# Kernel optimization log

Measured on AMD Instinct MI355X. Metric: run time of the kernel, lower is better.

Reference implementation:

```python
import jax, jax.numpy as jnp
import numpy as np

SCALE = 0.02
EPS = 1e-5


def setup_inputs() -> dict:
    key = jax.random.key(0)
    ks = jax.random.split(key, 11)
    C = 256
    inp = {
        "x": jax.random.normal(ks[0], (64, C, 28, 28), dtype=jnp.float32),
        "w1": jax.random.normal(ks[1], (C, C, 3, 3), dtype=jnp.float32) * 0.05,
        "g1": jax.random.uniform(ks[2], (C,), dtype=jnp.float32, minval=0.5, maxval=1.5),
        "b1": jax.random.normal(ks[3], (C,), dtype=jnp.float32) * 0.1,
        "m1": jax.random.normal(ks[4], (C,), dtype=jnp.float32) * 0.1,
        "v1": jax.random.uniform(ks[5], (C,), dtype=jnp.float32, minval=0.5, maxval=1.5),
        "w2": jax.random.normal(ks[6], (C, C, 3, 3), dtype=jnp.float32) * 0.05,
        "g2": jax.random.uniform(ks[7], (C,), dtype=jnp.float32, minval=0.5, maxval=1.5),
        "b2": jax.random.normal(ks[8], (C,), dtype=jnp.float32) * 0.1,
        "m2": jax.random.normal(ks[9], (C,), dtype=jnp.float32) * 0.1,
        "v2": jax.random.uniform(ks[10], (C,), dtype=jnp.float32, minval=0.5, maxval=1.5),
    }
    return inp


def _bin_conv3x3(x, w, stride=1):
    # 1-bit weight conv: sign(w)*scale, straight-through estimator for grads.
    wb = w + jax.lax.stop_gradient(jnp.sign(w) - w)
    y = jax.lax.conv_general_dilated(
        x, wb,
        window_strides=(stride, stride),
        padding=[(1, 1), (1, 1)],
        dimension_numbers=("NCHW", "OIHW", "NCHW"),
    )
    return y * SCALE


def _bn(x, g, b, m, v):
    # eval-mode batchnorm with running stats
    inv = g * jax.lax.rsqrt(v + EPS)  # [C]
    return x * inv[None, :, None, None] + (b - m * inv)[None, :, None, None]


def reference(x, w1, g1, b1, m1, v1, w2, g2, b2, m2, v2):
    out = jax.nn.relu(_bn(_bin_conv3x3(x, w1, 1), g1, b1, m1, v1))
    out = _bn(_bin_conv3x3(out, w2, 1), g2, b2, m2, v2)
    return jax.nn.relu(out + x)
```

## Files before the change

kernel.cpp:

```cpp
#include <hip/hip_runtime.h>

#define EPS_F 1e-5f
#define SCALE_F 0.02f

using short8  = __attribute__((ext_vector_type(8))) short;
using floatx4 = __attribute__((ext_vector_type(4))) float;

__device__ __forceinline__ unsigned short f2bf(float f) {
  unsigned u = __float_as_uint(f);
  return (unsigned short)((u + 0x7fffu + ((u >> 16) & 1u)) >> 16);
}

__global__ void prep_w(const float* __restrict__ w1, const float* __restrict__ w2,
                       unsigned short* __restrict__ ap1, unsigned short* __restrict__ ap2,
                       const float* g1, const float* b1, const float* m1, const float* v1,
                       const float* g2, const float* b2, const float* m2, const float* v2,
                       float* bnp) {
  const float* __restrict__ w = blockIdx.y ? w2 : w1;
  unsigned short* __restrict__ ap = blockIdx.y ? ap2 : ap1;
  int t = blockIdx.x * 256 + threadIdx.x;
  int off = t >> 13;
  int c8  = (t >> 8) & 31;
  int co  = t & 255;
  const float* ws = w + (size_t)(co * 256 + c8 * 8) * 9 + off;
  short8 o;
#pragma unroll
  for (int j = 0; j < 8; ++j) {
    float v = ws[j * 9];
    o[j] = (v > 0.f) ? (short)0x3F80 : ((v < 0.f) ? (short)0xBF80 : (short)0);
  }
  *(short8*)(ap + (size_t)t * 8) = o;
  if (blockIdx.x == 0 && blockIdx.y == 0) {
    int c = threadIdx.x;
    float i1 = g1[c] * rsqrtf(v1[c] + EPS_F);
    bnp[c]       = SCALE_F * i1;
    bnp[256 + c] = b1[c] - m1[c] * i1;
    float i2 = g2[c] * rsqrtf(v2[c] + EPS_F);
    bnp[512 + c] = SCALE_F * i2;
    bnp[768 + c] = b2[c] - m2[c] * i2;
  }
}

__global__ void prep_x(const float* __restrict__ x, unsigned short* __restrict__ xb,
                       unsigned short* __restrict__ abuf) {
  __shared__ float tile[28 * 260];
  int h = blockIdx.x;
  int n = blockIdx.y;
  int tid = threadIdx.x;
  const float* xs = x + ((size_t)n * 256) * 784 + h * 28;
  for (int u = tid; u < 1792; u += 256) {
    int ci = u / 7;
    int j  = u - ci * 7;
    floatx4 f = *(const floatx4*)&xs[(size_t)ci * 784 + j * 4];
    tile[(j * 4 + 0) * 260 + ci] = f[0];
    tile[(j * 4 + 1) * 260 + ci] = f[1];
    tile[(j * 4 + 2) * 260 + ci] = f[2];
    tile[(j * 4 + 3) * 260 + ci] = f[3];
  }
  __syncthreads();
  unsigned short* xd = xb + ((size_t)n * 900 + (h + 1) * 30 + 1) * 256;
  for (int u = tid; u < 1792; u += 256) {
    int w  = u >> 6;
    int c4 = u & 63;
    floatx4 f = *(const floatx4*)&tile[w * 260 + c4 * 4];
    ushort4 o;
    o.x = f2bf(f[0]); o.y = f2bf(f[1]); o.z = f2bf(f[2]); o.w = f2bf(f[3]);
    *(ushort4*)(xd + (size_t)w * 256 + c4 * 4) = o;
  }
  {
    int bufi = tid >> 7, side = (tid >> 6) & 1, c4 = tid & 63;
    unsigned short* bb = (bufi ? abuf : xb) + ((size_t)n * 900 + (h + 1) * 30 + side * 29) * 256;
    ushort4 z = {0, 0, 0, 0};
    *(ushort4*)(bb + c4 * 4) = z;
  }
  if (h == 0 || h == 27) {
    int row = (h == 0) ? 0 : 29;
    for (int u = tid; u < 3840; u += 256) {
      int bufi = u / 1920;
      int r    = u - bufi * 1920;
      int px   = r >> 6, c4 = r & 63;
      unsigned short* bb = (bufi ? abuf : xb) + ((size_t)n * 900 + row * 30 + px) * 256;
      ushort4 z = {0, 0, 0, 0};
      *(ushort4*)(bb + c4 * 4) = z;
    }
  }
}

template<int STAGE>
__global__ __launch_bounds__(256, 2) void bconv(
    const unsigned short* __restrict__ Bin,
    const unsigned short* __restrict__ Apack,
    const float* __restrict__ bnp,
    unsigned short* __restrict__ aout,
    const float* __restrict__ xres,
    float* __restrict__ out)
{
  __shared__ __align__(16) unsigned short Blds[180 * 64];

  const int tid  = threadIdx.x;
  const int lane = tid & 63;
  const int wv   = tid >> 6;
  const int quad = lane >> 4;
  const int l16  = lane & 15;
  const int spBlk = blockIdx.x;
  const int n     = blockIdx.y;

  const int prow0 = 4 * spBlk;
  const unsigned short* bsrc = Bin + ((size_t)n * 900 + prow0 * 30) * 256;
  const int coW = wv * 64;

  int pxS[7];
#pragma unroll
  for (int s = 0; s < 7; ++s) {
    int lm = s * 16 + l16;
    int hl = lm / 28;
    int w  = lm - hl * 28;
    pxS[s] = hl * 30 + w;
  }

  floatx4 acc[4][7];
#pragma unroll
  for (int c = 0; c < 4; ++c)
#pragma unroll
    for (int s = 0; s < 7; ++s)
      acc[c][s] = (floatx4){0.f, 0.f, 0.f, 0.f};

#pragma unroll 1
  for (int cb = 0; cb < 4; ++cb) {
    __syncthreads();
    for (int u = tid; u < 1440; u += 256) {
      int px = u >> 3, c = u & 7;
      const unsigned short* src = bsrc + (size_t)px * 256 + cb * 64 + c * 8;
      *(short8*)&Blds[(px << 6) + ((c ^ (px & 7)) << 3)] = *(const short8*)src;
    }
    __syncthreads();

    const int cq = cb * 8 + quad;
#pragma unroll 1
    for (int kh = 0; kh < 3; ++kh) {
#pragma unroll 1
      for (int kw = 0; kw < 3; ++kw) {
        const int D = kh * 30 + kw;
        const int chunk0 = (kh * 3 + kw) * 32 + cq;
#pragma unroll
        for (int half = 0; half < 2; ++half) {
          const int chunk = chunk0 + half * 4;
          const unsigned short* apb = Apack + ((size_t)(chunk * 256 + coW + l16)) * 8;
          short8 a0 = *(const short8*)(apb);
          short8 a1 = *(const short8*)(apb + 16 * 8);
          short8 a2 = *(const short8*)(apb + 32 * 8);
          short8 a3 = *(const short8*)(apb + 48 * 8);
          const int C = half * 4 + quad;
#pragma unroll
          for (int s = 0; s < 7; ++s) {
            int pe = pxS[s] + D;
            short8 b = *(const short8*)&Blds[(pe << 6) + ((C ^ (pe & 7)) << 3)];
            acc[0][s] = __builtin_amdgcn_mfma_f32_16x16x32_bf16(a0, b, acc[0][s], 0, 0, 0);
            acc[1][s] = __builtin_amdgcn_mfma_f32_16x16x32_bf16(a1, b, acc[1][s], 0, 0, 0);
            acc[2][s] = __builtin_amdgcn_mfma_f32_16x16x32_bf16(a2, b, acc[2][s], 0, 0, 0);
            acc[3][s] = __builtin_amdgcn_mfma_f32_16x16x32_bf16(a3, b, acc[3][s], 0, 0, 0);
          }
        }
      }
    }
  }

  if (STAGE == 1) {
#pragma unroll
    for (int c = 0; c < 4; ++c) {
      int co = coW + c * 16 + quad * 4;
      floatx4 As = *(const floatx4*)(bnp + co);
      floatx4 Bs = *(const floatx4*)(bnp + 256 + co);
#pragma unroll
      for (int s = 0; s < 7; ++s) {
        int lm = s * 16 + l16;
        int hl = lm / 28;
        int w  = lm - hl * 28;
        int pix = (prow0 + hl + 1) * 30 + w + 1;
        unsigned short* dst = aout + ((size_t)n * 900 + pix) * 256 + co;
        ushort4 o;
        o.x = f2bf(fmaxf(acc[c][s][0] * As[0] + Bs[0], 0.f));
        o.y = f2bf(fmaxf(acc[c][s][1] * As[1] + Bs[1], 0.f));
        o.z = f2bf(fmaxf(acc[c][s][2] * As[2] + Bs[2], 0.f));
        o.w = f2bf(fmaxf(acc[c][s][3] * As[3] + Bs[3], 0.f));
        *(ushort4*)dst = o;
      }
    }
  } else {
#pragma unroll
    for (int c = 0; c < 4; ++c) {
      int co = coW + c * 16 + quad * 4;
      floatx4 As = *(const floatx4*)(bnp + 512 + co);
      floatx4 Bs = *(const floatx4*)(bnp + 768 + co);
#pragma unroll
      for (int s = 0; s < 7; ++s) {
        int m = spBlk * 112 + s * 16 + l16;
#pragma unroll
        for (int r = 0; r < 4; ++r) {
          size_t oidx = ((size_t)n * 256 + co + r) * 784 + m;
          float v = acc[c][s][r] * As[r] + Bs[r] + xres[oidx];
          out[oidx] = fmaxf(v, 0.f);
        }
      }
    }
  }
}


extern "C" void kernel_launch(void* const* d_in, const int* in_sizes, int n_in,
                              void* d_out, int out_size, void* d_ws, size_t ws_size,
                              hipStream_t stream) {
  const float* x  = (const float*)d_in[0];
  const float* w1 = (const float*)d_in[1];
  const float* g1 = (const float*)d_in[2];
  const float* b1 = (const float*)d_in[3];
  const float* m1 = (const float*)d_in[4];
  const float* v1 = (const float*)d_in[5];
  const float* w2 = (const float*)d_in[6];
  const float* g2 = (const float*)d_in[7];
  const float* b2 = (const float*)d_in[8];
  const float* m2 = (const float*)d_in[9];
  const float* v2 = (const float*)d_in[10];
  float* out = (float*)d_out;

  char* ws = (char*)d_ws;
  const size_t PADBUF = (size_t)64 * 900 * 256 * 2;
  const size_t WPACK  = 589824ull * 2;
  unsigned short* xb   = (unsigned short*)ws;
  unsigned short* abuf = (unsigned short*)(ws + PADBUF);
  unsigned short* ap1  = (unsigned short*)(ws + 2 * PADBUF);
  unsigned short* ap2  = (unsigned short*)(ws + 2 * PADBUF + WPACK);
  float* bnp           = (float*)(ws + 2 * PADBUF + 2 * WPACK);

  prep_w<<<dim3(288, 2), 256, 0, stream>>>(w1, w2, ap1, ap2,
                                           g1, b1, m1, v1, g2, b2, m2, v2, bnp);
  prep_x<<<dim3(28, 64), 256, 0, stream>>>(x, xb, abuf);

  dim3 grid(7, 64);
  bconv<1><<<grid, 256, 0, stream>>>(xb,   ap1, bnp, abuf, nullptr, nullptr);
  bconv<2><<<grid, 256, 0, stream>>>(abuf, ap2, bnp, nullptr, x, out);
}
```

Measured before the change: 264.0 us.

## Stage conv1 epilogue through LDS for coalesced stores, simplify prep_x transpose

The stage-1 epilogue now writes BN+ReLU bf16 results into a padded shared-memory tile and then copies them to the padded activation buffer as 16-byte coalesced stores, replacing scattered 8-byte stores. prep_x drops its shared-memory transpose: each thread handles one channel and writes 2-byte bf16 values directly. The kw loop in the conv is also fully unrolled. The costs are a larger LDS footprint for stage 1, which may lower occupancy, and uncoalesced 2-byte stores in prep_x.

```diff
diff --git a/kernel.cpp b/kernel.cpp
--- a/kernel.cpp
+++ b/kernel.cpp
@@ -43,29 +43,17 @@
 
 __global__ void prep_x(const float* __restrict__ x, unsigned short* __restrict__ xb,
                        unsigned short* __restrict__ abuf) {
-  __shared__ float tile[28 * 260];
   int h = blockIdx.x;
   int n = blockIdx.y;
   int tid = threadIdx.x;
-  const float* xs = x + ((size_t)n * 256) * 784 + h * 28;
-  for (int u = tid; u < 1792; u += 256) {
-    int ci = u / 7;
-    int j  = u - ci * 7;
-    floatx4 f = *(const floatx4*)&xs[(size_t)ci * 784 + j * 4];
-    tile[(j * 4 + 0) * 260 + ci] = f[0];
-    tile[(j * 4 + 1) * 260 + ci] = f[1];
-    tile[(j * 4 + 2) * 260 + ci] = f[2];
-    tile[(j * 4 + 3) * 260 + ci] = f[3];
-  }
-  __syncthreads();
-  unsigned short* xd = xb + ((size_t)n * 900 + (h + 1) * 30 + 1) * 256;
-  for (int u = tid; u < 1792; u += 256) {
-    int w  = u >> 6;
-    int c4 = u & 63;
-    floatx4 f = *(const floatx4*)&tile[w * 260 + c4 * 4];
-    ushort4 o;
-    o.x = f2bf(f[0]); o.y = f2bf(f[1]); o.z = f2bf(f[2]); o.w = f2bf(f[3]);
-    *(ushort4*)(xd + (size_t)w * 256 + c4 * 4) = o;
+  const float* xs = x + ((size_t)n * 256 + tid) * 784 + h * 28;
+  unsigned short* xd = xb + ((size_t)n * 900 + (h + 1) * 30 + 1) * 256 + tid;
+#pragma unroll
+  for (int p4 = 0; p4 < 7; ++p4) {
+    floatx4 f = *(const floatx4*)(xs + p4 * 4);
+#pragma unroll
+    for (int k = 0; k < 4; ++k)
+      xd[(size_t)(p4 * 4 + k) * 256] = f2bf(f[k]);
   }
   {
     int bufi = tid >> 7, side = (tid >> 6) & 1, c4 = tid & 63;
@@ -95,7 +83,8 @@
     const float* __restrict__ xres,
     float* __restrict__ out)
 {
-  __shared__ __align__(16) unsigned short Blds[180 * 64];
+  __shared__ __align__(16) unsigned short smem[STAGE == 1 ? 29568 : 11520];
+  unsigned short* Blds = smem;
 
   const int tid  = threadIdx.x;
   const int lane = tid & 63;
@@ -138,7 +127,7 @@
     const int cq = cb * 8 + quad;
 #pragma unroll 1
     for (int kh = 0; kh < 3; ++kh) {
-#pragma unroll 1
+#pragma unroll
       for (int kw = 0; kw < 3; ++kw) {
         const int D = kh * 30 + kw;
         const int chunk0 = (kh * 3 + kw) * 32 + cq;
@@ -166,6 +155,7 @@
   }
 
   if (STAGE == 1) {
+    __syncthreads();
 #pragma unroll
     for (int c = 0; c < 4; ++c) {
       int co = coW + c * 16 + quad * 4;
@@ -173,18 +163,23 @@
       floatx4 Bs = *(const floatx4*)(bnp + 256 + co);
 #pragma unroll
       for (int s = 0; s < 7; ++s) {
-        int lm = s * 16 + l16;
-        int hl = lm / 28;
-        int w  = lm - hl * 28;
-        int pix = (prow0 + hl + 1) * 30 + w + 1;
-        unsigned short* dst = aout + ((size_t)n * 900 + pix) * 256 + co;
+        int px = s * 16 + l16;
         ushort4 o;
         o.x = f2bf(fmaxf(acc[c][s][0] * As[0] + Bs[0], 0.f));
         o.y = f2bf(fmaxf(acc[c][s][1] * As[1] + Bs[1], 0.f));
         o.z = f2bf(fmaxf(acc[c][s][2] * As[2] + Bs[2], 0.f));
         o.w = f2bf(fmaxf(acc[c][s][3] * As[3] + Bs[3], 0.f));
-        *(ushort4*)dst = o;
+        *(ushort4*)&smem[px * 264 + co] = o;
       }
+    }
+    __syncthreads();
+    unsigned short* dst0 = aout + ((size_t)n * 900 + (prow0 + 1) * 30 + 1) * 256;
+    for (int u = tid; u < 3584; u += 256) {
+      int px = u >> 5;
+      int c8 = (u & 31) * 8;
+      int r  = px / 28;
+      int w  = px - r * 28;
+      *(short8*)(dst0 + (size_t)(r * 30 + w) * 256 + c8) = *(const short8*)&smem[px * 264 + c8];
     }
   } else {
 #pragma unroll
```

Result: faster. 252.1 us (-4.5%).
